# Optimization experiments

Hardware: AMD Instinct MI355X
Metric: run time of the kernel (lower is better)

The kernel has to match this reference:

```python
import jax, jax.numpy as jnp
import numpy as np

H, DH, L, G = 4, 16, 6, 256


def _ln(x, eps=1e-6):
    m = x.mean(-1, keepdims=True)
    v = ((x - m) ** 2).mean(-1, keepdims=True)
    return (x - m) * jax.lax.rsqrt(v + eps)


def _sh(u):
    # real spherical harmonics l=0,1,2, 'component' normalization (e3nn style), unit input
    x, y, z = u[:, 0], u[:, 1], u[:, 2]
    s3, s15, s5 = 3.0 ** 0.5, 15.0 ** 0.5, 5.0 ** 0.5
    return jnp.stack([
        jnp.ones_like(x),
        s3 * x, s3 * y, s3 * z,
        s15 * x * y, s15 * y * z, (s5 / 2.0) * (3.0 * z * z - 1.0),
        s15 * x * z, (s15 / 2.0) * (x * x - y * y),
    ], axis=-1)


def _seg_softmax(logits, seg, n):
    m = jax.ops.segment_max(logits, seg, num_segments=n)
    ex = jnp.exp(logits - m[seg])
    s = jax.ops.segment_sum(ex, seg, num_segments=n)
    return ex / (s[seg] + 1e-9)


def setup_inputs() -> dict:
    key = jax.random.key(0)
    ks = jax.random.split(key, 24)
    N, E = 16384, 262144
    D = H * DH  # 64

    def w(k, shape, fan_in):
        return (jax.random.normal(k, shape, dtype=jnp.float32) / np.sqrt(fan_in)).astype(jnp.float32)

    inp = {
        'node_num': N,
        'edge_src': jax.random.randint(ks[0], (E,), 0, N, dtype=jnp.int32),
        'edge_dst': jax.random.randint(ks[1], (E,), 0, N, dtype=jnp.int32),
        'edge_vec': jax.random.normal(ks[2], (E, 3), dtype=jnp.float32) * 2.0,
        'batch': jnp.sort(jax.random.randint(ks[3], (N,), 0, G, dtype=jnp.int32)),
        'node_atom': jax.random.randint(ks[4], (N,), 0, 120, dtype=jnp.int32),
        'ele_embed_w': jax.random.normal(ks[5], (120, 32), dtype=jnp.float32) * 0.05,
        'W_embed': w(ks[6], (32, D), 32),
        'W_edge': w(ks[7], (32 + 32 + 9 + 64, D), 137),
        'Wq': w(ks[8], (L, D, D), D),
        'Wk': w(ks[9], (L, D, D), D),
        'Wv': w(ks[10], (L, D, D), D),
        'Wr1': w(ks[11], (L, 64, 64), 64),
        'Wr2': w(ks[12], (L, 64, H), 64),
        'Wo': w(ks[13], (L, D, D), D),
        'W1': w(ks[14], (L, D, 4 * D), D),
        'W2': w(ks[15], (L, 4 * D, D), 4 * D),
        'W_feat': w(ks[16], (D, 512), D),
        'hW1': w(ks[17], (512, 64), 512),
        'hb1': jnp.zeros((64,), jnp.float32),
        'hW2': w(ks[18], (64, 64), 64),
        'hb2': jnp.zeros((64,), jnp.float32),
        'hW3': w(ks[19], (64, 1), 64),
        'hb3': jnp.zeros((1,), jnp.float32),
    }
    return inp


def reference(node_num, edge_src, edge_dst, edge_vec, batch, node_atom,
              ele_embed_w, W_embed, W_edge, Wq, Wk, Wv, Wr1, Wr2, Wo, W1, W2,
              W_feat, hW1, hb1, hW2, hb2, hW3, hb3):
    N = int(node_num)
    E = edge_src.shape[0]

    # edge geometry: SH of permuted+normalized edge vector, gaussian RBF of length
    r = jnp.linalg.norm(edge_vec, axis=1)
    u = edge_vec[:, jnp.array([1, 2, 0])] / (r[:, None] + 1e-12)
    sh = _sh(u)                                   # [E, 9]
    centers = jnp.linspace(0.0, 10.0, 64, dtype=jnp.float32)
    width = 0.5 * 10.0 / 64.0
    rbf = jnp.exp(-((r[:, None] - centers) ** 2) / (2.0 * width * width))  # [E, 64]
    mask = r < 10.0                               # range_dis = [0, 10)

    # w2v path: atom embedding, edge features = cat(src, dst)
    nf = ele_embed_w[node_atom]                   # [N, 32]
    x = nf @ W_embed                              # [N, 64]
    e_ctx = jnp.concatenate([nf[edge_src], nf[edge_dst], sh, rbf], axis=-1)  # [E,137]
    e = e_ctx @ W_edge                            # [E, 64]

    for l in range(L):
        h = _ln(x)
        q = (h[edge_dst] @ Wq[l]).reshape(E, H, DH)
        src_in = h[edge_src] + e
        k = (src_in @ Wk[l]).reshape(E, H, DH)
        v = (src_in @ Wv[l]).reshape(E, H, DH)
        radial = jax.nn.silu(rbf @ Wr1[l]) @ Wr2[l]           # [E, H]
        logits = (q * k).sum(-1) / np.sqrt(DH) + radial        # [E, H]
        logits = jnp.where(mask[:, None], logits, -1e9)
        alpha = _seg_softmax(logits, edge_dst, N)              # softmax over in-edges
        msg = (alpha[..., None] * v).reshape(E, H * DH)
        agg = jax.ops.segment_sum(msg, edge_dst, num_segments=N)
        x = x + agg @ Wo[l]
        h2 = _ln(x)
        x = x + jax.nn.silu(h2 @ W1[l]) @ W2[l]

    feat = _ln(x @ W_feat)                        # [N, 512], irreps_feature = 512x0e
    hh = jax.nn.relu(_ln(feat @ hW1 + hb1))
    hh = jax.nn.relu(_ln(hh @ hW2 + hb2))
    energy = hh @ hW3 + hb3                       # [N, 1]
    pooled = jax.ops.segment_sum(energy, batch, num_segments=G) / np.sqrt(72.0)
    return pooled
```

## Files before the change

### kernel.cpp

```cpp
#include <hip/hip_runtime.h>

typedef short s8v __attribute__((ext_vector_type(8)));
typedef float f32x4 __attribute__((ext_vector_type(4)));
typedef unsigned short u16;

__device__ __forceinline__ float bf2f(u16 h){
  union { unsigned u; float f; } v; v.u = ((unsigned)h) << 16; return v.f;
}
__device__ __forceinline__ u16 f2bf(float f){
  union { float f; unsigned u; } v; v.f = f;
  unsigned u = v.u;
  return (u16)((u + 0x7fffu + ((u >> 16) & 1u)) >> 16);
}
#define MFMA(a,b,c) __builtin_amdgcn_mfma_f32_16x16x32_bf16((a),(b),(c),0,0,0)

#define WREDUCE64(s) { s += __shfl_xor(s,1); s += __shfl_xor(s,2); s += __shfl_xor(s,4); \
                       s += __shfl_xor(s,8); s += __shfl_xor(s,16); s += __shfl_xor(s,32); }
#define QREDUCE16(s) { s += __shfl_xor(s,1); s += __shfl_xor(s,2); s += __shfl_xor(s,4); s += __shfl_xor(s,8); }

__device__ __forceinline__ float quad_butterfly16(float* val, int c){
  float v8[8], v4[4], v2[2];
  #pragma unroll
  for(int t=0;t<8;t++){
    float sent = (c&1) ? val[2*t] : val[2*t+1];
    float got = __shfl_xor(sent, 1);
    v8[t] = ((c&1) ? val[2*t+1] : val[2*t]) + got;
  }
  #pragma unroll
  for(int t=0;t<4;t++){
    float sent = ((c>>1)&1) ? v8[2*t] : v8[2*t+1];
    float got = __shfl_xor(sent, 2);
    v4[t] = (((c>>1)&1) ? v8[2*t+1] : v8[2*t]) + got;
  }
  #pragma unroll
  for(int t=0;t<2;t++){
    float sent = ((c>>2)&1) ? v4[2*t] : v4[2*t+1];
    float got = __shfl_xor(sent, 4);
    v2[t] = (((c>>2)&1) ? v4[2*t+1] : v4[2*t]) + got;
  }
  float sent = ((c>>3)&1) ? v2[0] : v2[1];
  float got = __shfl_xor(sent, 8);
  return (((c>>3)&1) ? v2[1] : v2[0]) + got;
}

__global__ __launch_bounds__(256) void k_prep(const float* ele, const float* W_embed, const float* W_edge,
    const float* Wq, const float* Wk, const float* Wv, const float* Wr1, const float* Wo,
    const float* W1, const float* W2, const float* W_feat, const float* hW1, const float* hW2,
    u16* dst){
  int idx = blockIdx.x*256 + threadIdx.x;
  if(idx >= 405248) return;
  u16 v;
  if(idx < 3840){
    v = f2bf(ele[idx]);
  } else if(idx < 5888){
    int l = idx - 3840;
    int cI = l >> 5, rI = l & 31;
    v = f2bf(W_embed[rI*64 + cI]);
  } else if(idx < 16128){
    int l = idx - 5888;
    int cI = l / 160, rI = l - cI*160;
    v = (rI < 137) ? f2bf(W_edge[rI*64 + cI]) : (u16)0;
  } else if(idx < 139008){
    int l = idx - 16128;
    int which = l / 24576;
    int rem = l - which*24576;
    const float* src = (which==0)?Wq:(which==1)?Wk:(which==2)?Wv:(which==3)?Wr1:Wo;
    int b = rem >> 12;
    int r2 = rem & 4095;
    int cI = r2 >> 6, rI = r2 & 63;
    v = f2bf(src[b*4096 + rI*64 + cI]);
  } else if(idx < 237312){
    int l = idx - 139008;
    int b = l / 16384;
    int rem = l - b*16384;
    int cI = rem >> 6, rI = rem & 63;
    v = f2bf(W1[b*16384 + rI*256 + cI]);
  } else if(idx < 335616){
    int l = idx - 237312;
    int b = l / 16384;
    int rem = l - b*16384;
    int cI = rem >> 8, rI = rem & 255;
    v = f2bf(W2[b*16384 + rI*64 + cI]);
  } else if(idx < 368384){
    int l = idx - 335616;
    int cI = l >> 6, rI = l & 63;
    v = f2bf(W_feat[rI*512 + cI]);
  } else if(idx < 401152){
    int l = idx - 368384;
    int cI = l >> 9, rI = l & 511;
    v = f2bf(hW1[rI*64 + cI]);
  } else {
    int l = idx - 401152;
    int cI = l >> 6, rI = l & 63;
    v = f2bf(hW2[rI*64 + cI]);
  }
  dst[idx] = v;
}

__global__ __launch_bounds__(256) void k_count(const int* dstI, int* deg, int E){
  int tid = blockIdx.x*256 + threadIdx.x;
  if(tid < E) atomicAdd(&deg[dstI[tid]], 1);
}
__global__ __launch_bounds__(1024) void k_scan(const int* deg, int* rowptr, int* cursor, int N){
  __shared__ int wsum[17];
  int tid = threadIdx.x;
  int per = (N + 1023) >> 10;
  int base = tid * per;
  int s = 0;
  for(int i=0;i<per;i++){ int idx = base+i; if(idx < N) s += deg[idx]; }
  int lane = tid & 63, wid = tid >> 6;
  int inc = s;
  for(int d=1; d<64; d<<=1){
    int t = __shfl_up(inc, d);
    if(lane >= d) inc += t;
  }
  if(lane == 63) wsum[wid+1] = inc;
  if(tid == 0) wsum[0] = 0;
  __syncthreads();
  if(tid == 0){ for(int w=1; w<=16; w++) wsum[w] += wsum[w-1]; }
  __syncthreads();
  int run = inc - s + wsum[wid];
  for(int i=0;i<per;i++){
    int idx = base + i;
    if(idx < N){ rowptr[idx] = run; cursor[idx] = run; run += deg[idx]; }
  }
  if(tid == 1023) rowptr[N] = wsum[16];
}
__global__ __launch_bounds__(256) void k_scatter(const int* dstI, int* cursor, int* csr, int E){
  int tid = blockIdx.x*256 + threadIdx.x;
  if(tid < E){
    int p = atomicAdd(&cursor[dstI[tid]], 1);
    csr[p] = tid;
  }
}

__global__ __launch_bounds__(256) void k_edge_embed(const int* csr, const int* srcI, const int* dstI,
    const int* atom, const u16* ele, const float* evec, const u16* Bt,
    u16* ebf, float* r2, int* src2, int* dst2, int E){
  int wave = (blockIdx.x*blockDim.x + threadIdx.x) >> 6;
  int lane = threadIdx.x & 63;
  int row0 = wave*16; if(row0 >= E) return;
  int c = lane & 15, q = lane >> 4;
  int p = row0 + c;
  int e = csr[p];
  int sn = srcI[e], dn = dstI[e];
  float vx = evec[(size_t)e*3+0];
  float vy = evec[(size_t)e*3+1];
  float vz = evec[(size_t)e*3+2];
  float r = sqrtf(vx*vx + vy*vy + vz*vz);
  if(q == 0){ r2[p] = r; src2[p] = sn; dst2[p] = dn; }
  float inv = 1.f/(r + 1e-12f);
  float x = vy*inv, y = vz*inv, z = vx*inv;
  const float s3 = 1.7320508075688772f, s15 = 3.872983346207417f;
  const float s5h = 1.118033988749895f, s15h = 1.9364916731037085f;
  float sh[9];
  sh[0] = 1.f; sh[1] = s3*x; sh[2] = s3*y; sh[3] = s3*z;
  sh[4] = s15*x*y; sh[5] = s15*y*z; sh[6] = s5h*(3.f*z*z - 1.f);
  sh[7] = s15*x*z; sh[8] = s15h*(x*x - y*y);
  s8v a[5];
  a[0] = *reinterpret_cast<const s8v*>(ele + (size_t)atom[sn]*32 + q*8);
  a[1] = *reinterpret_cast<const s8v*>(ele + (size_t)atom[dn]*32 + q*8);
  #pragma unroll
  for(int j=0;j<8;j++){
    int col = 64 + q*8 + j;
    u16 v;
    if(q == 0)            v = f2bf(sh[j]);
    else if(col < 73)     v = f2bf(sh[8]);
    else { float d = r - (10.f/63.f)*(float)(col-73); v = f2bf(__expf(-81.92f*d*d)); }
    a[2][j] = (short)v;
  }
  #pragma unroll
  for(int j=0;j<8;j++){
    float d = r - (10.f/63.f)*(float)(23 + q*8 + j);
    a[3][j] = (short)f2bf(__expf(-81.92f*d*d));
  }
  #pragma unroll
  for(int j=0;j<8;j++){
    int col = 128 + q*8 + j;
    u16 v = 0;
    if(col < 137){ float d = r - (10.f/63.f)*(float)(col-73); v = f2bf(__expf(-81.92f*d*d)); }
    a[4][j] = (short)v;
  }
  #pragma unroll
  for(int ct=0; ct<4; ct++){
    f32x4 acc = {0.f,0.f,0.f,0.f};
    #pragma unroll
    for(int kc=0; kc<5; kc++){
      s8v b = *reinterpret_cast<const s8v*>(Bt + (ct*16+c)*160 + kc*32 + q*8);
      acc = MFMA(a[kc], b, acc);
    }
    #pragma unroll
    for(int r_=0;r_<4;r_++) ebf[(size_t)(row0+q*4+r_)*64 + ct*16 + c] = f2bf(acc[r_]);
  }
}

#define RG 4096
#define RGROWS 4112
__global__ __launch_bounds__(256) void k_radtab(const u16* Wr1T, const float* Wr2, float* radtab){
  int wave = (blockIdx.x*256 + threadIdx.x) >> 6;
  int lane = threadIdx.x & 63;
  int row0 = wave*16; if(row0 >= RGROWS) return;
  int c = lane & 15, q = lane >> 4;
  float re = (10.f/RG)*(float)(row0 + c);
  s8v r0, r1;
  #pragma unroll
  for(int j=0;j<8;j++){
    float d0 = re - (10.f/63.f)*(float)(q*8+j);
    float d1 = re - (10.f/63.f)*(float)(32+q*8+j);
    r0[j] = (short)f2bf(__expf(-81.92f*d0*d0));
    r1[j] = (short)f2bf(__expf(-81.92f*d1*d1));
  }
  for(int l=0; l<6; l++){
    const u16* W1l = Wr1T + l*4096;
    const float4* wr2v = reinterpret_cast<const float4*>(Wr2 + l*256);
    float val[16];
    #pragma unroll
    for(int i=0;i<16;i++) val[i] = 0.f;
    #pragma unroll
    for(int ct=0; ct<4; ct++){
      s8v bw0 = *reinterpret_cast<const s8v*>(W1l + (ct*16+c)*64 + q*8);
      s8v bw1 = *reinterpret_cast<const s8v*>(W1l + (ct*16+c)*64 + 32 + q*8);
      f32x4 hacc = {0.f,0.f,0.f,0.f};
      hacc = MFMA(r0, bw0, hacc); hacc = MFMA(r1, bw1, hacc);
      float4 w2 = wr2v[ct*16 + c];
      #pragma unroll
      for(int r=0;r<4;r++){
        float y = hacc[r];
        float sv = y / (1.f + __expf(-y));
        val[r*4+0] += sv * w2.x;
        val[r*4+1] += sv * w2.y;
        val[r*4+2] += sv * w2.z;
        val[r*4+3] += sv * w2.w;
      }
    }
    float fin = quad_butterfly16(val, c);
    int row = row0 + q*4 + (c>>2);
    if(row <= RG)
      radtab[(size_t)l*RGROWS*4 + (size_t)row0*4 + lane] = fin;
  }
}

__global__ __launch_bounds__(256) void k_pre(const int* atom, const u16* ele, const u16* WembT,
    const u16* WqT0, float* xb, u16* hbf, float* Qt, int M){
  __shared__ u16 ldsH[4][16*72];
  int widL = threadIdx.x >> 6;
  int wave = (blockIdx.x*256 + threadIdx.x) >> 6;
  int lane = threadIdx.x & 63;
  int row0 = wave*16; if(row0 >= M) return;
  int c = lane & 15, q = lane >> 4;
  u16* LH = ldsH[widL];
  int at = atom[row0 + c];
  s8v a = *reinterpret_cast<const s8v*>(ele + (size_t)at*32 + q*8);
  float nx[4][4];
  #pragma unroll
  for(int ct=0; ct<4; ct++){
    s8v b = *reinterpret_cast<const s8v*>(WembT + (ct*16+c)*32 + q*8);
    f32x4 acc = {0.f,0.f,0.f,0.f};
    acc = MFMA(a, b, acc);
    #pragma unroll
    for(int r=0;r<4;r++){
      xb[(size_t)(row0+q*4+r)*64 + ct*16 + c] = acc[r];
      nx[ct][r] = acc[r];
    }
  }
  #pragma unroll
  for(int r=0;r<4;r++){
    float s = nx[0][r]+nx[1][r]+nx[2][r]+nx[3][r];
    QREDUCE16(s);
    float m = s*(1.f/64.f);
    float vv = 0.f;
    #pragma unroll
    for(int ct=0;ct<4;ct++){ float d = nx[ct][r]-m; vv += d*d; }
    QREDUCE16(vv);
    float rs = rsqrtf(vv*(1.f/64.f) + 1e-6f);
    #pragma unroll
    for(int ct=0;ct<4;ct++){
      u16 hb = f2bf((nx[ct][r]-m)*rs);
      hbf[(size_t)(row0+q*4+r)*64 + ct*16 + c] = hb;
      LH[(q*4+r)*72 + ct*16 + c] = hb;
    }
  }
  s8v h0 = *reinterpret_cast<const s8v*>(LH + c*72 + q*8);
  s8v h1 = *reinterpret_cast<const s8v*>(LH + c*72 + 32 + q*8);
  #pragma unroll
  for(int ct=0; ct<4; ct++){
    s8v b0 = *reinterpret_cast<const s8v*>(WqT0 + (ct*16+c)*64 + q*8);
    s8v b1 = *reinterpret_cast<const s8v*>(WqT0 + (ct*16+c)*64 + 32 + q*8);
    f32x4 acc = {0.f,0.f,0.f,0.f};
    acc = MFMA(h0, b0, acc);
    acc = MFMA(h1, b1, acc);
    #pragma unroll
    for(int r=0;r<4;r++) Qt[(size_t)(row0+q*4+r)*64 + c*4 + ct] = acc[r];
  }
}

__global__ __launch_bounds__(256) void k_kvrad(const u16* hbf, const u16* ebf,
    const int* src2, const int* dst2, const float* Qt, const float* r2, const float* radtab,
    const u16* WkT, const u16* WvT, u16* vbf, float* exb, int E){
  int wave = (blockIdx.x*256 + threadIdx.x) >> 6;
  int lane = threadIdx.x & 63;
  int base0 = wave*32;
  if(base0 >= E) return;
  int c = lane & 15, q = lane >> 4;
  s8v a0[2], a1[2];
  #pragma unroll
  for(int t=0;t<2;t++){
    int row0 = base0 + t*16;
    int sr = src2[row0 + c];
    s8v h0 = *reinterpret_cast<const s8v*>(hbf + (size_t)sr*64 + q*8);
    s8v h1 = *reinterpret_cast<const s8v*>(hbf + (size_t)sr*64 + 32 + q*8);
    s8v e0 = *reinterpret_cast<const s8v*>(ebf + (size_t)(row0+c)*64 + q*8);
    s8v e1 = *reinterpret_cast<const s8v*>(ebf + (size_t)(row0+c)*64 + 32 + q*8);
    #pragma unroll
    for(int j=0;j<8;j++){
      a0[t][j] = (short)f2bf(bf2f((u16)h0[j]) + bf2f((u16)e0[j]));
      a1[t][j] = (short)f2bf(bf2f((u16)h1[j]) + bf2f((u16)e1[j]));
    }
  }
  const float4* QtV = reinterpret_cast<const float4*>(Qt);
  float4 qv[2][4];
  #pragma unroll
  for(int t=0;t<2;t++)
    #pragma unroll
    for(int r=0;r<4;r++){
      int dr = dst2[base0 + t*16 + q*4 + r];
      qv[t][r] = QtV[(size_t)dr*16 + c];
    }
  float val[2][16];
  #pragma unroll
  for(int t=0;t<2;t++)
    #pragma unroll
    for(int i=0;i<16;i++) val[t][i] = 0.f;
  #pragma unroll
  for(int ct=0; ct<4; ct++){
    s8v bk0 = *reinterpret_cast<const s8v*>(WkT + (ct*16+c)*64 + q*8);
    s8v bk1 = *reinterpret_cast<const s8v*>(WkT + (ct*16+c)*64 + 32 + q*8);
    s8v bv0 = *reinterpret_cast<const s8v*>(WvT + (ct*16+c)*64 + q*8);
    s8v bv1 = *reinterpret_cast<const s8v*>(WvT + (ct*16+c)*64 + 32 + q*8);
    #pragma unroll
    for(int t=0;t<2;t++){
      int row0 = base0 + t*16;
      f32x4 kacc = {0.f,0.f,0.f,0.f};
      kacc = MFMA(a0[t], bk0, kacc); kacc = MFMA(a1[t], bk1, kacc);
      f32x4 vacc = {0.f,0.f,0.f,0.f};
      vacc = MFMA(a0[t], bv0, vacc); vacc = MFMA(a1[t], bv1, vacc);
      #pragma unroll
      for(int r=0;r<4;r++){
        vbf[(size_t)row0*64 + (r*4+ct)*64 + q*16 + c] = f2bf(vacc[r]);
        float qc = (ct==0)?qv[t][r].x:(ct==1)?qv[t][r].y:(ct==2)?qv[t][r].z:qv[t][r].w;
        val[t][r*4+ct] += 0.25f * kacc[r] * qc;
      }
    }
  }
  #pragma unroll
  for(int t=0;t<2;t++){
    int row0 = base0 + t*16;
    float qk = quad_butterfly16(val[t], c);
    int row = row0 + q*4 + (c>>2);
    float re = r2[row];
    float tt = re * ((float)RG/10.f);
    tt = fminf(fmaxf(tt, 0.f), (float)RG - 0.0001f);
    int i0 = (int)tt;
    float fr = tt - (float)i0;
    int h = c & 3;
    float lo = radtab[(size_t)i0*4 + h];
    float hi = radtab[(size_t)(i0+1)*4 + h];
    float logit = qk + lo + (hi - lo)*fr;
    exb[(size_t)row0*4 + lane] = (re < 10.f) ? __expf(logit) : 0.f;
  }
}

__global__ __launch_bounds__(256) void k_agg(const int* rowptr, const float* exb, const u16* vbf, u16* aggbf, int N){
  int wave = (blockIdx.x*256 + threadIdx.x) >> 6;
  int lane = threadIdx.x & 63;
  if(wave >= N) return;
  int s0 = rowptr[wave], s1 = rowptr[wave+1];
  float s[4] = {0.f,0.f,0.f,0.f};
  for(int p = s0 + lane; p < s1; p += 64){
    float4 ev = *reinterpret_cast<const float4*>(exb + (size_t)p*4);
    s[0] += ev.x; s[1] += ev.y; s[2] += ev.z; s[3] += ev.w;
  }
  #pragma unroll
  for(int i=0;i<4;i++){ WREDUCE64(s[i]); }
  int ep = lane >> 4, cc = lane & 15;
  int hh = cc >> 2;
  int swz = hh*64 + (cc&3)*4;
  float inv = 1.f/(s[hh] + 1e-9f);
  float a0=0.f, a1=0.f, a2=0.f, a3=0.f;
  for(int p = s0 + ep; p < s1; p += 4){
    int t = p & 15;
    size_t base = (size_t)(p & ~15)*64 + (size_t)((t&3)*256) + (size_t)((t>>2)*16) + swz;
    ushort4 v4 = *reinterpret_cast<const ushort4*>(vbf + base);
    float ex = exb[(size_t)p*4 + hh];
    a0 += ex*bf2f(v4.x); a1 += ex*bf2f(v4.y); a2 += ex*bf2f(v4.z); a3 += ex*bf2f(v4.w);
  }
  a0 += __shfl_xor(a0,16); a0 += __shfl_xor(a0,32);
  a1 += __shfl_xor(a1,16); a1 += __shfl_xor(a1,32);
  a2 += __shfl_xor(a2,16); a2 += __shfl_xor(a2,32);
  a3 += __shfl_xor(a3,16); a3 += __shfl_xor(a3,32);
  if(ep == 0){
    ushort4 o;
    o.x = f2bf(a0*inv); o.y = f2bf(a1*inv); o.z = f2bf(a2*inv); o.w = f2bf(a3*inv);
    *reinterpret_cast<ushort4*>(aggbf + (size_t)wave*64 + cc*4) = o;
  }
}

__global__ __launch_bounds__(256) void k_mega(const u16* aggbf, const u16* WoT, float* x,
    const u16* W1T, const u16* W2T, const u16* WqTn, float* Qt, u16* hbf, u16* xbf,
    int writex, int haveQ, int M){
  __shared__ u16 ldsH[4][16*72];
  __shared__ u16 ldsT[4][16*264];
  int widL = threadIdx.x >> 6;
  int wave = (blockIdx.x*256 + threadIdx.x) >> 6;
  int lane = threadIdx.x & 63;
  int row0 = wave*16; if(row0 >= M) return;
  int c = lane & 15, q = lane >> 4;
  u16* LH = ldsH[widL];
  u16* LT = ldsT[widL];
  {
    s8v a0 = *reinterpret_cast<const s8v*>(aggbf + (size_t)(row0+c)*64 + q*8);
    s8v a1 = *reinterpret_cast<const s8v*>(aggbf + (size_t)(row0+c)*64 + 32 + q*8);
    float nx[4][4];
    #pragma unroll
    for(int ct=0; ct<4; ct++){
      s8v b0 = *reinterpret_cast<const s8v*>(WoT + (ct*16+c)*64 + q*8);
      s8v b1 = *reinterpret_cast<const s8v*>(WoT + (ct*16+c)*64 + 32 + q*8);
      f32x4 acc = {0.f,0.f,0.f,0.f};
      acc = MFMA(a0, b0, acc);
      acc = MFMA(a1, b1, acc);
      #pragma unroll
      for(int r=0;r<4;r++){
        size_t idx = (size_t)(row0+q*4+r)*64 + ct*16 + c;
        float t = x[idx] + acc[r];
        x[idx] = t;
        nx[ct][r] = t;
      }
    }
    #pragma unroll
    for(int r=0;r<4;r++){
      float s = nx[0][r]+nx[1][r]+nx[2][r]+nx[3][r];
      QREDUCE16(s);
      float m = s*(1.f/64.f);
      float vv = 0.f;
      #pragma unroll
      for(int ct=0;ct<4;ct++){ float d = nx[ct][r]-m; vv += d*d; }
      QREDUCE16(vv);
      float rs = rsqrtf(vv*(1.f/64.f) + 1e-6f);
      #pragma unroll
      for(int ct=0;ct<4;ct++)
        LH[(q*4+r)*72 + ct*16 + c] = f2bf((nx[ct][r]-m)*rs);
    }
  }
  __syncthreads();
  {
    s8v h0 = *reinterpret_cast<const s8v*>(LH + c*72 + q*8);
    s8v h1 = *reinterpret_cast<const s8v*>(LH + c*72 + 32 + q*8);
    #pragma unroll
    for(int ct=0; ct<16; ct++){
      s8v b0 = *reinterpret_cast<const s8v*>(W1T + (ct*16+c)*64 + q*8);
      s8v b1 = *reinterpret_cast<const s8v*>(W1T + (ct*16+c)*64 + 32 + q*8);
      f32x4 acc = {0.f,0.f,0.f,0.f};
      acc = MFMA(h0, b0, acc);
      acc = MFMA(h1, b1, acc);
      #pragma unroll
      for(int r=0;r<4;r++){
        float y = acc[r];
        LT[(q*4+r)*264 + ct*16 + c] = f2bf(y / (1.f + __expf(-y)));
      }
    }
  }
  __syncthreads();
  {
    s8v a[8];
    #pragma unroll
    for(int kc=0; kc<8; kc++)
      a[kc] = *reinterpret_cast<const s8v*>(LT + c*264 + kc*32 + q*8);
    float nx[4][4];
    #pragma unroll
    for(int ct=0; ct<4; ct++){
      f32x4 acc = {0.f,0.f,0.f,0.f};
      #pragma unroll
      for(int kc=0; kc<8; kc++){
        s8v b = *reinterpret_cast<const s8v*>(W2T + (ct*16+c)*256 + kc*32 + q*8);
        acc = MFMA(a[kc], b, acc);
      }
      #pragma unroll
      for(int r=0;r<4;r++){
        size_t idx = (size_t)(row0+q*4+r)*64 + ct*16 + c;
        float t = x[idx] + acc[r];
        x[idx] = t;
        nx[ct][r] = t;
        if(writex) xbf[idx] = f2bf(t);
      }
    }
    #pragma unroll
    for(int r=0;r<4;r++){
      float s = nx[0][r]+nx[1][r]+nx[2][r]+nx[3][r];
      QREDUCE16(s);
      float m = s*(1.f/64.f);
      float vv = 0.f;
      #pragma unroll
      for(int ct=0;ct<4;ct++){ float d = nx[ct][r]-m; vv += d*d; }
      QREDUCE16(vv);
      float rs = rsqrtf(vv*(1.f/64.f) + 1e-6f);
      #pragma unroll
      for(int ct=0;ct<4;ct++){
        u16 hb = f2bf((nx[ct][r]-m)*rs);
        hbf[(size_t)(row0+q*4+r)*64 + ct*16 + c] = hb;
        LH[(q*4+r)*72 + ct*16 + c] = hb;
      }
    }
  }
  if(haveQ){
    s8v h0 = *reinterpret_cast<const s8v*>(LH + c*72 + q*8);
    s8v h1 = *reinterpret_cast<const s8v*>(LH + c*72 + 32 + q*8);
    #pragma unroll
    for(int ct=0; ct<4; ct++){
      s8v b0 = *reinterpret_cast<const s8v*>(WqTn + (ct*16+c)*64 + q*8);
      s8v b1 = *reinterpret_cast<const s8v*>(WqTn + (ct*16+c)*64 + 32 + q*8);
      f32x4 acc = {0.f,0.f,0.f,0.f};
      acc = MFMA(h0, b0, acc);
      acc = MFMA(h1, b1, acc);
      #pragma unroll
      for(int r=0;r<4;r++) Qt[(size_t)(row0+q*4+r)*64 + c*4 + ct] = acc[r];
    }
  }
}

__global__ __launch_bounds__(256) void k_feat_ln(const u16* A, const u16* Bt, u16* out, int M){
  int wave = (blockIdx.x*256 + threadIdx.x) >> 6;
  int lane = threadIdx.x & 63;
  int row0 = wave*16; if(row0 >= M) return;
  int c = lane & 15, q = lane >> 4;
  s8v a0 = *reinterpret_cast<const s8v*>(A + (size_t)(row0+c)*64 + q*8);
  s8v a1 = *reinterpret_cast<const s8v*>(A + (size_t)(row0+c)*64 + 32 + q*8);
  float fa[32][4];
  #pragma unroll
  for(int ct=0; ct<32; ct++){
    s8v b0 = *reinterpret_cast<const s8v*>(Bt + (ct*16+c)*64 + q*8);
    s8v b1 = *reinterpret_cast<const s8v*>(Bt + (ct*16+c)*64 + 32 + q*8);
    f32x4 acc = {0.f,0.f,0.f,0.f};
    acc = MFMA(a0, b0, acc);
    acc = MFMA(a1, b1, acc);
    #pragma unroll
    for(int r=0;r<4;r++) fa[ct][r] = acc[r];
  }
  #pragma unroll
  for(int r=0;r<4;r++){
    float s = 0.f;
    #pragma unroll
    for(int ct=0;ct<32;ct++) s += fa[ct][r];
    QREDUCE16(s);
    float m = s*(1.f/512.f);
    float vv = 0.f;
    #pragma unroll
    for(int ct=0;ct<32;ct++){ float d = fa[ct][r]-m; vv += d*d; }
    QREDUCE16(vv);
    float rs = rsqrtf(vv*(1.f/512.f) + 1e-6f);
    #pragma unroll
    for(int ct=0;ct<32;ct++)
      out[(size_t)(row0+q*4+r)*512 + ct*16 + c] = f2bf((fa[ct][r]-m)*rs);
  }
}

__global__ __launch_bounds__(256) void k_head1_ln(const u16* A, const u16* Bt, const float* hb, u16* out, int M){
  int wave = (blockIdx.x*256 + threadIdx.x) >> 6;
  int lane = threadIdx.x & 63;
  int row0 = wave*16; if(row0 >= M) return;
  int c = lane & 15, q = lane >> 4;
  s8v a[16];
  #pragma unroll
  for(int kc=0; kc<16; kc++)
    a[kc] = *reinterpret_cast<const s8v*>(A + (size_t)(row0+c)*512 + kc*32 + q*8);
  float y[4][4];
  #pragma unroll
  for(int ct=0; ct<4; ct++){
    f32x4 acc = {0.f,0.f,0.f,0.f};
    #pragma unroll
    for(int kc=0; kc<16; kc++){
      s8v b = *reinterpret_cast<const s8v*>(Bt + (size_t)(ct*16+c)*512 + kc*32 + q*8);
      acc = MFMA(a[kc], b, acc);
    }
    float bi = hb[ct*16+c];
    #pragma unroll
    for(int r=0;r<4;r++) y[ct][r] = acc[r] + bi;
  }
  #pragma unroll
  for(int r=0;r<4;r++){
    float s = y[0][r]+y[1][r]+y[2][r]+y[3][r];
    QREDUCE16(s);
    float m = s*(1.f/64.f);
    float vv = 0.f;
    #pragma unroll
    for(int ct=0;ct<4;ct++){ float d = y[ct][r]-m; vv += d*d; }
    QREDUCE16(vv);
    float rs = rsqrtf(vv*(1.f/64.f) + 1e-6f);
    #pragma unroll
    for(int ct=0;ct<4;ct++)
      out[(size_t)(row0+q*4+r)*64 + ct*16 + c] = f2bf(fmaxf((y[ct][r]-m)*rs, 0.f));
  }
}

__global__ __launch_bounds__(256) void k_head2_energy(const u16* A, const u16* Bt, const float* hb,
    const float* hW3, const float* hb3, const int* batch, float* pooled, int M){
  int wave = (blockIdx.x*256 + threadIdx.x) >> 6;
  int lane = threadIdx.x & 63;
  int row0 = wave*16; if(row0 >= M) return;
  int c = lane & 15, q = lane >> 4;
  s8v a0 = *reinterpret_cast<const s8v*>(A + (size_t)(row0+c)*64 + q*8);
  s8v a1 = *reinterpret_cast<const s8v*>(A + (size_t)(row0+c)*64 + 32 + q*8);
  float y[4][4];
  #pragma unroll
  for(int ct=0; ct<4; ct++){
    s8v b0 = *reinterpret_cast<const s8v*>(Bt + (ct*16+c)*64 + q*8);
    s8v b1 = *reinterpret_cast<const s8v*>(Bt + (ct*16+c)*64 + 32 + q*8);
    f32x4 acc = {0.f,0.f,0.f,0.f};
    acc = MFMA(a0, b0, acc);
    acc = MFMA(a1, b1, acc);
    float bi = hb[ct*16+c];
    #pragma unroll
    for(int r=0;r<4;r++) y[ct][r] = acc[r] + bi;
  }
  float w3[4];
  #pragma unroll
  for(int ct=0;ct<4;ct++) w3[ct] = hW3[ct*16+c];
  float ep[4];
  #pragma unroll
  for(int r=0;r<4;r++){
    float s = y[0][r]+y[1][r]+y[2][r]+y[3][r];
    QREDUCE16(s);
    float m = s*(1.f/64.f);
    float vv = 0.f;
    #pragma unroll
    for(int ct=0;ct<4;ct++){ float d = y[ct][r]-m; vv += d*d; }
    QREDUCE16(vv);
    float rs = rsqrtf(vv*(1.f/64.f) + 1e-6f);
    float e = 0.f;
    #pragma unroll
    for(int ct=0;ct<4;ct++) e += fmaxf((y[ct][r]-m)*rs, 0.f) * w3[ct];
    QREDUCE16(e);
    ep[r] = e;
  }
  if(c < 4){
    float ev = (c==0)?ep[0]:(c==1)?ep[1]:(c==2)?ep[2]:ep[3];
    int row = row0 + q*4 + c;
    atomicAdd(&pooled[batch[row]], ev + hb3[0]);
  }
}

__global__ __launch_bounds__(256) void k_out(const float* pooled, float* out, int G){
  int tid = blockIdx.x*256 + threadIdx.x;
  if(tid < G) out[tid] = pooled[tid] * 0.11785113019775793f;
}

extern "C" void kernel_launch(void* const* d_in, const int* in_sizes, int n_in,
                              void* d_out, int out_size, void* d_ws, size_t ws_size,
                              hipStream_t stream){
  const int*   edge_src  = (const int*)d_in[1];
  const int*   edge_dst  = (const int*)d_in[2];
  const float* edge_vec  = (const float*)d_in[3];
  const int*   batch     = (const int*)d_in[4];
  const int*   node_atom = (const int*)d_in[5];
  const float* ele    = (const float*)d_in[6];
  const float* W_embed= (const float*)d_in[7];
  const float* W_edge = (const float*)d_in[8];
  const float* Wq = (const float*)d_in[9];
  const float* Wk = (const float*)d_in[10];
  const float* Wv = (const float*)d_in[11];
  const float* Wr1= (const float*)d_in[12];
  const float* Wr2= (const float*)d_in[13];
  const float* Wo = (const float*)d_in[14];
  const float* W1 = (const float*)d_in[15];
  const float* W2 = (const float*)d_in[16];
  const float* W_feat=(const float*)d_in[17];
  const float* hW1= (const float*)d_in[18];
  const float* hb1= (const float*)d_in[19];
  const float* hW2= (const float*)d_in[20];
  const float* hb2= (const float*)d_in[21];
  const float* hW3= (const float*)d_in[22];
  const float* hb3= (const float*)d_in[23];
  (void)n_in; (void)ws_size;

  const int E = in_sizes[1];
  const int N = in_sizes[4];
  const int G = out_size;

  char* base = (char*)d_ws;
  size_t off = 0;
  #define ALLOC(ty, name, count) ty* name = (ty*)(base + off); off = (off + (size_t)(count)*sizeof(ty) + 255) & ~(size_t)255;
  ALLOC(float, r2,    E)
  ALLOC(int,   src2,  E)
  ALLOC(int,   dst2,  E)
  ALLOC(u16,   ebf,   (size_t)E*64)
  ALLOC(u16,   vbf,   (size_t)E*64)
  ALLOC(float, exb,   (size_t)E*4)
  ALLOC(float, radtab,(size_t)6*RGROWS*4)
  ALLOC(u16,   hbf,   (size_t)N*64)
  ALLOC(u16,   aggbf, (size_t)N*64)
  ALLOC(u16,   xbf,   (size_t)N*64)
  ALLOC(float, Qt,    (size_t)N*64)
  ALLOC(float, xb,    (size_t)N*64)
  ALLOC(int,   deg,   N)
  ALLOC(int,   rowptr,N+1)
  ALLOC(int,   cursor,N)
  ALLOC(int,   csr,   E)
  ALLOC(float, pooled,G)
  ALLOC(u16, ele_bf, 120*32)
  ALLOC(u16, WembT, 64*32)
  ALLOC(u16, WedgeT,64*160)
  ALLOC(u16, WqT,  6*64*64)
  ALLOC(u16, WkT,  6*64*64)
  ALLOC(u16, WvT,  6*64*64)
  ALLOC(u16, Wr1T, 6*64*64)
  ALLOC(u16, WoT,  6*64*64)
  ALLOC(u16, W1T,  6*256*64)
  ALLOC(u16, W2T,  6*64*256)
  ALLOC(u16, WfT,  512*64)
  ALLOC(u16, hW1T, 64*512)
  ALLOC(u16, hW2T, 64*64)
  #undef ALLOC
  u16* featbf = ebf;
  u16* hh1    = (u16*)exb;

  auto cdiv = [](int a, int b){ return (a + b - 1)/b; };

  k_prep<<<cdiv(405248,256),256,0,stream>>>(ele, W_embed, W_edge, Wq, Wk, Wv, Wr1, Wo,
                                            W1, W2, W_feat, hW1, hW2, ele_bf);

  hipMemsetAsync(deg, 0, (size_t)N*sizeof(int), stream);
  hipMemsetAsync(pooled, 0, (size_t)G*sizeof(float), stream);

  k_count<<<cdiv(E,256),256,0,stream>>>(edge_dst, deg, E);
  k_scan<<<1,1024,0,stream>>>(deg, rowptr, cursor, N);
  k_scatter<<<cdiv(E,256),256,0,stream>>>(edge_dst, cursor, csr, E);
  k_edge_embed<<<E/64, 256, 0, stream>>>(csr, edge_src, edge_dst, node_atom, ele_bf, edge_vec,
                                         WedgeT, ebf, r2, src2, dst2, E);
  k_radtab<<<cdiv(RGROWS*4,256),256,0,stream>>>(Wr1T, Wr2, radtab);
  k_pre<<<N/64,256,0,stream>>>(node_atom, ele_bf, WembT, WqT, xb, hbf, Qt, N);

  for(int l=0; l<6; l++){
    k_kvrad<<<E/128,256,0,stream>>>(hbf, ebf, src2, dst2, Qt, r2, radtab + (size_t)l*RGROWS*4,
                                    WkT + l*4096, WvT + l*4096, vbf, exb, E);
    k_agg<<<cdiv(N,4),256,0,stream>>>(rowptr, exb, vbf, aggbf, N);
    k_mega<<<N/64,256,0,stream>>>(aggbf, WoT + l*4096, xb,
                                  W1T + l*16384, W2T + l*16384,
                                  WqT + ((l<5)?(l+1):0)*4096, Qt, hbf, xbf,
                                  (l==5)?1:0, (l<5)?1:0, N);
  }

  k_feat_ln<<<N/64,256,0,stream>>>(xbf, WfT, featbf, N);
  k_head1_ln<<<N/64,256,0,stream>>>(featbf, hW1T, hb1, hh1, N);
  k_head2_energy<<<N/64,256,0,stream>>>(hh1, hW2T, hb2, hW3, hb3, batch, pooled, N);
  k_out<<<cdiv(G,256),256,0,stream>>>(pooled, (float*)d_out, G);
}
```

Before: 674.9 us.

## Fuse output head kernels, widen edge-embed tiles, drop syncs in mega kernel

Merges the three output-head kernels (feature LN, head1 LN, head2 energy) into one kernel that keeps intermediates in per-wave LDS, so the 512-wide feature tensor no longer makes a round trip through global memory and two launches disappear. The edge-embedding kernel now has each wave process two 16-row tiles, which reuses the loaded weight fragments across both tiles. Two __syncthreads in the mega kernel are removed on the assumption that each wave only touches its own LDS rows. That last assumption needs per-wave LDS ownership, and the new larger LDS footprint in the tail kernel may lower occupancy.

```diff
diff --git a/kernel.cpp b/kernel.cpp
--- a/kernel.cpp
+++ b/kernel.cpp
@@ -137,60 +137,69 @@
 __global__ __launch_bounds__(256) void k_edge_embed(const int* csr, const int* srcI, const int* dstI,
     const int* atom, const u16* ele, const float* evec, const u16* Bt,
     u16* ebf, float* r2, int* src2, int* dst2, int E){
-  int wave = (blockIdx.x*blockDim.x + threadIdx.x) >> 6;
+  int wave = (blockIdx.x*256 + threadIdx.x) >> 6;
   int lane = threadIdx.x & 63;
-  int row0 = wave*16; if(row0 >= E) return;
+  int base0 = wave*32; if(base0 >= E) return;
   int c = lane & 15, q = lane >> 4;
-  int p = row0 + c;
-  int e = csr[p];
-  int sn = srcI[e], dn = dstI[e];
-  float vx = evec[(size_t)e*3+0];
-  float vy = evec[(size_t)e*3+1];
-  float vz = evec[(size_t)e*3+2];
-  float r = sqrtf(vx*vx + vy*vy + vz*vz);
-  if(q == 0){ r2[p] = r; src2[p] = sn; dst2[p] = dn; }
-  float inv = 1.f/(r + 1e-12f);
-  float x = vy*inv, y = vz*inv, z = vx*inv;
-  const float s3 = 1.7320508075688772f, s15 = 3.872983346207417f;
-  const float s5h = 1.118033988749895f, s15h = 1.9364916731037085f;
-  float sh[9];
-  sh[0] = 1.f; sh[1] = s3*x; sh[2] = s3*y; sh[3] = s3*z;
-  sh[4] = s15*x*y; sh[5] = s15*y*z; sh[6] = s5h*(3.f*z*z - 1.f);
-  sh[7] = s15*x*z; sh[8] = s15h*(x*x - y*y);
-  s8v a[5];
-  a[0] = *reinterpret_cast<const s8v*>(ele + (size_t)atom[sn]*32 + q*8);
-  a[1] = *reinterpret_cast<const s8v*>(ele + (size_t)atom[dn]*32 + q*8);
-  #pragma unroll
-  for(int j=0;j<8;j++){
-    int col = 64 + q*8 + j;
-    u16 v;
-    if(q == 0)            v = f2bf(sh[j]);
-    else if(col < 73)     v = f2bf(sh[8]);
-    else { float d = r - (10.f/63.f)*(float)(col-73); v = f2bf(__expf(-81.92f*d*d)); }
-    a[2][j] = (short)v;
-  }
-  #pragma unroll
-  for(int j=0;j<8;j++){
-    float d = r - (10.f/63.f)*(float)(23 + q*8 + j);
-    a[3][j] = (short)f2bf(__expf(-81.92f*d*d));
-  }
-  #pragma unroll
-  for(int j=0;j<8;j++){
-    int col = 128 + q*8 + j;
-    u16 v = 0;
-    if(col < 137){ float d = r - (10.f/63.f)*(float)(col-73); v = f2bf(__expf(-81.92f*d*d)); }
-    a[4][j] = (short)v;
+  s8v a[2][5];
+  #pragma unroll
+  for(int t=0;t<2;t++){
+    int row0 = base0 + t*16;
+    int p = row0 + c;
+    int e = csr[p];
+    int sn = srcI[e], dn = dstI[e];
+    float vx = evec[(size_t)e*3+0];
+    float vy = evec[(size_t)e*3+1];
+    float vz = evec[(size_t)e*3+2];
+    float r = sqrtf(vx*vx + vy*vy + vz*vz);
+    if(q == 0){ r2[p] = r; src2[p] = sn; dst2[p] = dn; }
+    float inv = 1.f/(r + 1e-12f);
+    float x = vy*inv, y = vz*inv, z = vx*inv;
+    const float s3 = 1.7320508075688772f, s15 = 3.872983346207417f;
+    const float s5h = 1.118033988749895f, s15h = 1.9364916731037085f;
+    float sh[9];
+    sh[0] = 1.f; sh[1] = s3*x; sh[2] = s3*y; sh[3] = s3*z;
+    sh[4] = s15*x*y; sh[5] = s15*y*z; sh[6] = s5h*(3.f*z*z - 1.f);
+    sh[7] = s15*x*z; sh[8] = s15h*(x*x - y*y);
+    a[t][0] = *reinterpret_cast<const s8v*>(ele + (size_t)atom[sn]*32 + q*8);
+    a[t][1] = *reinterpret_cast<const s8v*>(ele + (size_t)atom[dn]*32 + q*8);
+    #pragma unroll
+    for(int j=0;j<8;j++){
+      int col = 64 + q*8 + j;
+      u16 v;
+      if(q == 0)            v = f2bf(sh[j]);
+      else if(col < 73)     v = f2bf(sh[8]);
+      else { float d = r - (10.f/63.f)*(float)(col-73); v = f2bf(__expf(-81.92f*d*d)); }
+      a[t][2][j] = (short)v;
+    }
+    #pragma unroll
+    for(int j=0;j<8;j++){
+      float d = r - (10.f/63.f)*(float)(23 + q*8 + j);
+      a[t][3][j] = (short)f2bf(__expf(-81.92f*d*d));
+    }
+    #pragma unroll
+    for(int j=0;j<8;j++){
+      int col = 128 + q*8 + j;
+      u16 v = 0;
+      if(col < 137){ float d = r - (10.f/63.f)*(float)(col-73); v = f2bf(__expf(-81.92f*d*d)); }
+      a[t][4][j] = (short)v;
+    }
   }
   #pragma unroll
   for(int ct=0; ct<4; ct++){
-    f32x4 acc = {0.f,0.f,0.f,0.f};
-    #pragma unroll
-    for(int kc=0; kc<5; kc++){
-      s8v b = *reinterpret_cast<const s8v*>(Bt + (ct*16+c)*160 + kc*32 + q*8);
-      acc = MFMA(a[kc], b, acc);
-    }
-    #pragma unroll
-    for(int r_=0;r_<4;r_++) ebf[(size_t)(row0+q*4+r_)*64 + ct*16 + c] = f2bf(acc[r_]);
+    s8v b[5];
+    #pragma unroll
+    for(int kc=0; kc<5; kc++)
+      b[kc] = *reinterpret_cast<const s8v*>(Bt + (ct*16+c)*160 + kc*32 + q*8);
+    #pragma unroll
+    for(int t=0;t<2;t++){
+      int row0 = base0 + t*16;
+      f32x4 acc = {0.f,0.f,0.f,0.f};
+      #pragma unroll
+      for(int kc=0; kc<5; kc++) acc = MFMA(a[t][kc], b[kc], acc);
+      #pragma unroll
+      for(int r_=0;r_<4;r_++) ebf[(size_t)(row0+q*4+r_)*64 + ct*16 + c] = f2bf(acc[r_]);
+    }
   }
 }
 
@@ -451,7 +460,6 @@
         LH[(q*4+r)*72 + ct*16 + c] = f2bf((nx[ct][r]-m)*rs);
     }
   }
-  __syncthreads();
   {
     s8v h0 = *reinterpret_cast<const s8v*>(LH + c*72 + q*8);
     s8v h1 = *reinterpret_cast<const s8v*>(LH + c*72 + 32 + q*8);
@@ -469,7 +477,6 @@
       }
     }
   }
-  __syncthreads();
   {
     s8v a[8];
     #pragma unroll
@@ -527,124 +534,119 @@
   }
 }
 
-__global__ __launch_bounds__(256) void k_feat_ln(const u16* A, const u16* Bt, u16* out, int M){
+__global__ __launch_bounds__(256) void k_tail(const u16* xbf, const u16* WfT,
+    const u16* hW1T, const float* hb1, const u16* hW2T, const float* hb2,
+    const float* hW3, const float* hb3, const int* batch, float* pooled, int M){
+  __shared__ u16 ldsF[4][16*522];
+  __shared__ u16 ldsH[4][16*72];
+  int widL = threadIdx.x >> 6;
   int wave = (blockIdx.x*256 + threadIdx.x) >> 6;
   int lane = threadIdx.x & 63;
   int row0 = wave*16; if(row0 >= M) return;
   int c = lane & 15, q = lane >> 4;
-  s8v a0 = *reinterpret_cast<const s8v*>(A + (size_t)(row0+c)*64 + q*8);
-  s8v a1 = *reinterpret_cast<const s8v*>(A + (size_t)(row0+c)*64 + 32 + q*8);
-  float fa[32][4];
-  #pragma unroll
-  for(int ct=0; ct<32; ct++){
-    s8v b0 = *reinterpret_cast<const s8v*>(Bt + (ct*16+c)*64 + q*8);
-    s8v b1 = *reinterpret_cast<const s8v*>(Bt + (ct*16+c)*64 + 32 + q*8);
-    f32x4 acc = {0.f,0.f,0.f,0.f};
-    acc = MFMA(a0, b0, acc);
-    acc = MFMA(a1, b1, acc);
-    #pragma unroll
-    for(int r=0;r<4;r++) fa[ct][r] = acc[r];
-  }
-  #pragma unroll
-  for(int r=0;r<4;r++){
-    float s = 0.f;
-    #pragma unroll
-    for(int ct=0;ct<32;ct++) s += fa[ct][r];
-    QREDUCE16(s);
-    float m = s*(1.f/512.f);
-    float vv = 0.f;
-    #pragma unroll
-    for(int ct=0;ct<32;ct++){ float d = fa[ct][r]-m; vv += d*d; }
-    QREDUCE16(vv);
-    float rs = rsqrtf(vv*(1.f/512.f) + 1e-6f);
-    #pragma unroll
-    for(int ct=0;ct<32;ct++)
-      out[(size_t)(row0+q*4+r)*512 + ct*16 + c] = f2bf((fa[ct][r]-m)*rs);
-  }
-}
-
-__global__ __launch_bounds__(256) void k_head1_ln(const u16* A, const u16* Bt, const float* hb, u16* out, int M){
-  int wave = (blockIdx.x*256 + threadIdx.x) >> 6;
-  int lane = threadIdx.x & 63;
-  int row0 = wave*16; if(row0 >= M) return;
-  int c = lane & 15, q = lane >> 4;
-  s8v a[16];
-  #pragma unroll
-  for(int kc=0; kc<16; kc++)
-    a[kc] = *reinterpret_cast<const s8v*>(A + (size_t)(row0+c)*512 + kc*32 + q*8);
-  float y[4][4];
-  #pragma unroll
-  for(int ct=0; ct<4; ct++){
-    f32x4 acc = {0.f,0.f,0.f,0.f};
-    #pragma unroll
-    for(int kc=0; kc<16; kc++){
-      s8v b = *reinterpret_cast<const s8v*>(Bt + (size_t)(ct*16+c)*512 + kc*32 + q*8);
-      acc = MFMA(a[kc], b, acc);
-    }
-    float bi = hb[ct*16+c];
-    #pragma unroll
-    for(int r=0;r<4;r++) y[ct][r] = acc[r] + bi;
-  }
-  #pragma unroll
-  for(int r=0;r<4;r++){
-    float s = y[0][r]+y[1][r]+y[2][r]+y[3][r];
-    QREDUCE16(s);
-    float m = s*(1.f/64.f);
-    float vv = 0.f;
-    #pragma unroll
-    for(int ct=0;ct<4;ct++){ float d = y[ct][r]-m; vv += d*d; }
-    QREDUCE16(vv);
-    float rs = rsqrtf(vv*(1.f/64.f) + 1e-6f);
-    #pragma unroll
-    for(int ct=0;ct<4;ct++)
-      out[(size_t)(row0+q*4+r)*64 + ct*16 + c] = f2bf(fmaxf((y[ct][r]-m)*rs, 0.f));
-  }
-}
-
-__global__ __launch_bounds__(256) void k_head2_energy(const u16* A, const u16* Bt, const float* hb,
-    const float* hW3, const float* hb3, const int* batch, float* pooled, int M){
-  int wave = (blockIdx.x*256 + threadIdx.x) >> 6;
-  int lane = threadIdx.x & 63;
-  int row0 = wave*16; if(row0 >= M) return;
-  int c = lane & 15, q = lane >> 4;
-  s8v a0 = *reinterpret_cast<const s8v*>(A + (size_t)(row0+c)*64 + q*8);
-  s8v a1 = *reinterpret_cast<const s8v*>(A + (size_t)(row0+c)*64 + 32 + q*8);
-  float y[4][4];
-  #pragma unroll
-  for(int ct=0; ct<4; ct++){
-    s8v b0 = *reinterpret_cast<const s8v*>(Bt + (ct*16+c)*64 + q*8);
-    s8v b1 = *reinterpret_cast<const s8v*>(Bt + (ct*16+c)*64 + 32 + q*8);
-    f32x4 acc = {0.f,0.f,0.f,0.f};
-    acc = MFMA(a0, b0, acc);
-    acc = MFMA(a1, b1, acc);
-    float bi = hb[ct*16+c];
-    #pragma unroll
-    for(int r=0;r<4;r++) y[ct][r] = acc[r] + bi;
-  }
-  float w3[4];
-  #pragma unroll
-  for(int ct=0;ct<4;ct++) w3[ct] = hW3[ct*16+c];
-  float ep[4];
-  #pragma unroll
-  for(int r=0;r<4;r++){
-    float s = y[0][r]+y[1][r]+y[2][r]+y[3][r];
-    QREDUCE16(s);
-    float m = s*(1.f/64.f);
-    float vv = 0.f;
-    #pragma unroll
-    for(int ct=0;ct<4;ct++){ float d = y[ct][r]-m; vv += d*d; }
-    QREDUCE16(vv);
-    float rs = rsqrtf(vv*(1.f/64.f) + 1e-6f);
-    float e = 0.f;
-    #pragma unroll
-    for(int ct=0;ct<4;ct++) e += fmaxf((y[ct][r]-m)*rs, 0.f) * w3[ct];
-    QREDUCE16(e);
-    ep[r] = e;
-  }
-  if(c < 4){
-    float ev = (c==0)?ep[0]:(c==1)?ep[1]:(c==2)?ep[2]:ep[3];
-    int row = row0 + q*4 + c;
-    atomicAdd(&pooled[batch[row]], ev + hb3[0]);
+  u16* LF = ldsF[widL];
+  u16* LH = ldsH[widL];
+  {
+    s8v a0 = *reinterpret_cast<const s8v*>(xbf + (size_t)(row0+c)*64 + q*8);
+    s8v a1 = *reinterpret_cast<const s8v*>(xbf + (size_t)(row0+c)*64 + 32 + q*8);
+    float fa[32][4];
+    #pragma unroll
+    for(int ct=0; ct<32; ct++){
+      s8v b0 = *reinterpret_cast<const s8v*>(WfT + (ct*16+c)*64 + q*8);
+      s8v b1 = *reinterpret_cast<const s8v*>(WfT + (ct*16+c)*64 + 32 + q*8);
+      f32x4 acc = {0.f,0.f,0.f,0.f};
+      acc = MFMA(a0, b0, acc);
+      acc = MFMA(a1, b1, acc);
+      #pragma unroll
+      for(int r=0;r<4;r++) fa[ct][r] = acc[r];
+    }
+    #pragma unroll
+    for(int r=0;r<4;r++){
+      float s = 0.f;
+      #pragma unroll
+      for(int ct=0;ct<32;ct++) s += fa[ct][r];
+      QREDUCE16(s);
+      float m = s*(1.f/512.f);
+      float vv = 0.f;
+      #pragma unroll
+      for(int ct=0;ct<32;ct++){ float d = fa[ct][r]-m; vv += d*d; }
+      QREDUCE16(vv);
+      float rs = rsqrtf(vv*(1.f/512.f) + 1e-6f);
+      #pragma unroll
+      for(int ct=0;ct<32;ct++)
+        LF[(q*4+r)*522 + ct*16 + c] = f2bf((fa[ct][r]-m)*rs);
+    }
+  }
+  {
+    float y[4][4];
+    #pragma unroll
+    for(int ct=0; ct<4; ct++){
+      f32x4 acc = {0.f,0.f,0.f,0.f};
+      #pragma unroll
+      for(int kc=0; kc<16; kc++){
+        s8v af = *reinterpret_cast<const s8v*>(LF + c*522 + kc*32 + q*8);
+        s8v b = *reinterpret_cast<const s8v*>(hW1T + (size_t)(ct*16+c)*512 + kc*32 + q*8);
+        acc = MFMA(af, b, acc);
+      }
+      float bi = hb1[ct*16+c];
+      #pragma unroll
+      for(int r=0;r<4;r++) y[ct][r] = acc[r] + bi;
+    }
+    #pragma unroll
+    for(int r=0;r<4;r++){
+      float s = y[0][r]+y[1][r]+y[2][r]+y[3][r];
+      QREDUCE16(s);
+      float m = s*(1.f/64.f);
+      float vv = 0.f;
+      #pragma unroll
+      for(int ct=0;ct<4;ct++){ float d = y[ct][r]-m; vv += d*d; }
+      QREDUCE16(vv);
+      float rs = rsqrtf(vv*(1.f/64.f) + 1e-6f);
+      #pragma unroll
+      for(int ct=0;ct<4;ct++)
+        LH[(q*4+r)*72 + ct*16 + c] = f2bf(fmaxf((y[ct][r]-m)*rs, 0.f));
+    }
+  }
+  {
+    s8v a0 = *reinterpret_cast<const s8v*>(LH + c*72 + q*8);
+    s8v a1 = *reinterpret_cast<const s8v*>(LH + c*72 + 32 + q*8);
+    float y[4][4];
+    #pragma unroll
+    for(int ct=0; ct<4; ct++){
+      s8v b0 = *reinterpret_cast<const s8v*>(hW2T + (ct*16+c)*64 + q*8);
+      s8v b1 = *reinterpret_cast<const s8v*>(hW2T + (ct*16+c)*64 + 32 + q*8);
+      f32x4 acc = {0.f,0.f,0.f,0.f};
+      acc = MFMA(a0, b0, acc);
+      acc = MFMA(a1, b1, acc);
+      float bi = hb2[ct*16+c];
+      #pragma unroll
+      for(int r=0;r<4;r++) y[ct][r] = acc[r] + bi;
+    }
+    float w3[4];
+    #pragma unroll
+    for(int ct=0;ct<4;ct++) w3[ct] = hW3[ct*16+c];
+    float ep[4];
+    #pragma unroll
+    for(int r=0;r<4;r++){
+      float s = y[0][r]+y[1][r]+y[2][r]+y[3][r];
+      QREDUCE16(s);
+      float m = s*(1.f/64.f);
+      float vv = 0.f;
+      #pragma unroll
+      for(int ct=0;ct<4;ct++){ float d = y[ct][r]-m; vv += d*d; }
+      QREDUCE16(vv);
+      float rs = rsqrtf(vv*(1.f/64.f) + 1e-6f);
+      float e = 0.f;
+      #pragma unroll
+      for(int ct=0;ct<4;ct++) e += fmaxf((y[ct][r]-m)*rs, 0.f) * w3[ct];
+      QREDUCE16(e);
+      ep[r] = e;
+    }
+    if(c < 4){
+      float ev = (c==0)?ep[0]:(c==1)?ep[1]:(c==2)?ep[2]:ep[3];
+      int row = row0 + q*4 + c;
+      atomicAdd(&pooled[batch[row]], ev + hb3[0]);
+    }
   }
 }
 
@@ -719,8 +721,6 @@
   ALLOC(u16, hW1T, 64*512)
   ALLOC(u16, hW2T, 64*64)
   #undef ALLOC
-  u16* featbf = ebf;
-  u16* hh1    = (u16*)exb;
 
   auto cdiv = [](int a, int b){ return (a + b - 1)/b; };
 
@@ -733,8 +733,8 @@
   k_count<<<cdiv(E,256),256,0,stream>>>(edge_dst, deg, E);
   k_scan<<<1,1024,0,stream>>>(deg, rowptr, cursor, N);
   k_scatter<<<cdiv(E,256),256,0,stream>>>(edge_dst, cursor, csr, E);
-  k_edge_embed<<<E/64, 256, 0, stream>>>(csr, edge_src, edge_dst, node_atom, ele_bf, edge_vec,
-                                         WedgeT, ebf, r2, src2, dst2, E);
+  k_edge_embed<<<E/128, 256, 0, stream>>>(csr, edge_src, edge_dst, node_atom, ele_bf, edge_vec,
+                                          WedgeT, ebf, r2, src2, dst2, E);
   k_radtab<<<cdiv(RGROWS*4,256),256,0,stream>>>(Wr1T, Wr2, radtab);
   k_pre<<<N/64,256,0,stream>>>(node_atom, ele_bf, WembT, WqT, xb, hbf, Qt, N);
 
@@ -748,8 +748,6 @@
                                   (l==5)?1:0, (l<5)?1:0, N);
   }
 
-  k_feat_ln<<<N/64,256,0,stream>>>(xbf, WfT, featbf, N);
-  k_head1_ln<<<N/64,256,0,stream>>>(featbf, hW1T, hb1, hh1, N);
-  k_head2_energy<<<N/64,256,0,stream>>>(hh1, hW2T, hb2, hW3, hb3, batch, pooled, N);
+  k_tail<<<N/64,256,0,stream>>>(xbf, WfT, hW1T, hb1, hW2T, hb2, hW3, hb3, batch, pooled, N);
   k_out<<<cdiv(G,256),256,0,stream>>>(pooled, (float*)d_out, G);
 }
```

Result: faster. 660.2 us (-2.2%).
